# Kernel tuning notes

Hardware: AMD Instinct MI355X
Metric: run time of the kernel (lower is better)

The kernel has to match this reference:

```python
import jax, jax.numpy as jnp
import numpy as np

B, T, F, U, L = 64, 512, 256, 1024, 3
LN_EPS = 1e-12  # tf.contrib.layers.layer_norm default


def setup_inputs() -> dict:
    key = jax.random.key(0)
    ks = jax.random.split(key, 8)

    def w(k, shape):
        return jax.random.normal(k, shape, jnp.float32) / np.float32(np.sqrt(shape[0]))

    return {
        "input": jax.random.normal(ks[0], (B, T, F), jnp.float32),
        "conditioned_lst": jax.random.randint(ks[1], (T,), 0, 2).astype(bool),
        # LSTM layer 0: input = feature F, layers 1..2: input = U
        "W0": w(ks[2], (F + U, 4 * U)), "b0": jnp.zeros((4 * U,), jnp.float32),
        "W1": w(ks[3], (2 * U, 4 * U)), "b1": jnp.zeros((4 * U,), jnp.float32),
        "W2": w(ks[4], (2 * U, 4 * U)), "b2": jnp.zeros((4 * U,), jnp.float32),
        # output dense projection back to feature dim
        "Wd": w(ks[5], (U, F)), "bd": jnp.zeros((F,), jnp.float32),
        # layer norm params
        "gamma": jnp.ones((F,), jnp.float32), "beta": jnp.zeros((F,), jnp.float32),
    }


def _lstm_cell(x, h, c, W, b):
    # BasicLSTMCell: gates in (i, j, f, o) order, forget_bias = 1.0
    z = jnp.dot(jnp.concatenate([x, h], axis=-1), W) + b
    i, j, f, o = jnp.split(z, 4, axis=-1)
    c_new = c * jax.nn.sigmoid(f + 1.0) + jax.nn.sigmoid(i) * jnp.tanh(j)
    h_new = jax.nn.sigmoid(o) * jnp.tanh(c_new)
    return h_new, c_new


def reference(input, conditioned_lst, W0, b0, W1, b1, W2, b2, Wd, bd, gamma, beta):
    Ws, bs = [W0, W1, W2], [b0, b1, b2]
    xs = (jnp.arange(T), jnp.swapaxes(input, 0, 1), conditioned_lst)  # time-major
    carry0 = (jnp.zeros((L, B, U), input.dtype),  # h per layer
              jnp.zeros((L, B, U), input.dtype),  # c per layer
              jnp.zeros((B, F), input.dtype))     # previous emit

    def step(carry, xt):
        hs, cs, prev_emit = carry
        t, x_t, cond_t = xt
        # auto-conditioning: teacher-force on conditioned steps (and step 0)
        x = jnp.where(jnp.logical_or(t == 0, cond_t), x_t, prev_emit)
        new_h, new_c = [], []
        for l in range(L):
            h, c = _lstm_cell(x, hs[l], cs[l], Ws[l], bs[l])
            new_h.append(h)
            new_c.append(c)
            x = h
        y = jnp.dot(x, Wd) + bd  # dense projection [B, F]
        mu = jnp.mean(y, axis=-1, keepdims=True)
        var = jnp.mean(jnp.square(y - mu), axis=-1, keepdims=True)
        y = (y - mu) * jax.lax.rsqrt(var + LN_EPS) * gamma + beta
        emit = jax.nn.relu(y)
        return (jnp.stack(new_h), jnp.stack(new_c), emit), emit

    _, outs = jax.lax.scan(step, carry0, xs)  # [T, B, F]
    return jnp.swapaxes(outs, 0, 1)  # [B, T, F]
```

## Files before the change

### kernel.cpp

```cpp
#include <hip/hip_runtime.h>
#include <math.h>

#define B 64
#define T 512
#define F 256
#define U 1024
#define NBLK 256
#define NTH 512
#define WPAD 68

typedef unsigned short ushort_t;
typedef __attribute__((ext_vector_type(8))) _Float16 f16x8_t;
typedef __attribute__((ext_vector_type(4))) float f32x4_t;

static const size_t OFF_STATS= 0;
static const size_t OFF_COND = 4096;
static const size_t OFF_BAR  = 6144;
static const size_t OFF_H2B  = 7424;
static const size_t OFF_HS   = 269568;
static const size_t OFF_XS   = 1056000;
static const size_t OFF_PW0  = 1088768;
static const size_t OFF_PW1  = 11574528;
static const size_t OFF_PW2  = 28351744;
static const size_t ZERO_BYTES = OFF_PW0;

__device__ __forceinline__ float sigm(float x) {
    return 1.0f / (1.0f + __expf(-x));
}

__device__ __forceinline__ ushort_t f2h(float x) {
    _Float16 h = (_Float16)x;
    union { _Float16 h; ushort_t u; } v; v.h = h;
    return v.u;
}

__device__ __forceinline__ void store_uc_u16(ushort_t* p, ushort_t v) {
    asm volatile("global_store_short %0, %1, off sc0 sc1"
                 :: "v"(p), "v"((unsigned)v) : "memory");
}
__device__ __forceinline__ void store_uc_f32(float* p, float v) {
    asm volatile("global_store_dword %0, %1, off sc0 sc1"
                 :: "v"(p), "v"(v) : "memory");
}
__device__ __forceinline__ void store_uc_b64(void* p, unsigned long long v) {
    asm volatile("global_store_dwordx2 %0, %1, off sc0 sc1"
                 :: "v"(p), "v"(v) : "memory");
}
__device__ __forceinline__ void drain_vmem() {
    asm volatile("s_waitcnt vmcnt(0)" ::: "memory");
}
__device__ __forceinline__ void wait_vm0() {
    asm volatile("s_waitcnt vmcnt(0)" ::: "memory");
    __builtin_amdgcn_sched_barrier(0);
}

__device__ __forceinline__ void phase_sync(int* bar, int epoch, int g) {
    drain_vmem();
    __syncthreads();
    if (threadIdx.x == 0) {
        const int sub = g & 7;
        const int prev = __hip_atomic_fetch_add(bar + sub * 16, 1,
                                                __ATOMIC_RELAXED, __HIP_MEMORY_SCOPE_AGENT);
        if (prev == epoch * 32 - 1) {
            const int pm = __hip_atomic_fetch_add(bar + 128, 1,
                                                  __ATOMIC_RELAXED, __HIP_MEMORY_SCOPE_AGENT);
            if (pm == epoch * 8 - 1) {
                #pragma unroll
                for (int i = 0; i < 8; ++i)
                    __hip_atomic_store(bar + 144 + i * 16, epoch, __ATOMIC_RELAXED,
                                       __HIP_MEMORY_SCOPE_AGENT);
            }
        }
        int* myrelay = bar + 144 + sub * 16;
        int spins = 0;
        while (__hip_atomic_load(myrelay, __ATOMIC_RELAXED,
                                 __HIP_MEMORY_SCOPE_AGENT) < epoch) {
            __builtin_amdgcn_s_sleep(2);
            if ((++spins & 63) == 0)
                (void)__hip_atomic_load(myrelay, __ATOMIC_ACQUIRE,
                                        __HIP_MEMORY_SCOPE_AGENT);
        }
    }
    __syncthreads();
}

__global__ void prep_kernel(const unsigned char* __restrict__ condraw,
                            const float* __restrict__ input,
                            unsigned char* __restrict__ wsb) {
    __shared__ int s_not_int32;
    const int tid = threadIdx.x;
    if (tid == 0) s_not_int32 = 0;
    __syncthreads();
    if (tid < 512 && (tid & 3) != 0) {
        if (condraw[tid] != 0) s_not_int32 = 1;
    }
    __syncthreads();
    const int is32 = (s_not_int32 == 0);
    int* condw = (int*)(wsb + OFF_COND);
    if (tid < 512) {
        int cv = is32 ? ((const int*)condraw)[tid] : (int)condraw[tid];
        condw[tid] = (cv != 0) ? 1 : 0;
    }
    ushort_t* xs = (ushort_t*)(wsb + OFF_XS);
    for (int i = tid; i < B * F; i += blockDim.x) {
        const int b = i >> 8, f = i & 255;
        xs[(size_t)(((f >> 2) << 6) + b) * 4 + (f & 3)] =
            f2h(input[(size_t)b * (T * F) + f]);
    }
}

__global__ void repack_kernel(const float* __restrict__ W0,
                              const float* __restrict__ W1,
                              const float* __restrict__ W2,
                              unsigned char* __restrict__ wsb) {
    ushort_t* P0 = (ushort_t*)(wsb + OFF_PW0);
    ushort_t* P1 = (ushort_t*)(wsb + OFF_PW1);
    ushort_t* P2 = (ushort_t*)(wsb + OFF_PW2);
    const size_t stride = (size_t)gridDim.x * blockDim.x;
    const size_t tid = (size_t)blockIdx.x * blockDim.x + threadIdx.x;
    const size_t N0 = (size_t)256 * 40 * 512;
    const size_t N12 = (size_t)256 * 64 * 512;
    for (size_t i = tid; i < N0; i += stride) {
        const int g = (int)(i / 20480);
        const int r = (int)(i % 20480);
        const int kt = r >> 9, s = r & 511, L = s >> 3, j = s & 7;
        const int k = kt * 32 + ((L >> 4) << 3) + j;
        const int n = L & 15;
        const int col = ((n >> 2) << 10) + (g << 2) + (n & 3);
        P0[i] = f2h(W0[(size_t)k * 4096 + col]);
    }
    for (size_t i = tid; i < N12; i += stride) {
        const int g = (int)(i / 32768);
        const int r = (int)(i % 32768);
        const int kt = r >> 9, s = r & 511, L = s >> 3, j = s & 7;
        const int k = kt * 32 + ((L >> 4) << 3) + j;
        const int n = L & 15;
        const int col = ((n >> 2) << 10) + (g << 2) + (n & 3);
        const size_t src = (size_t)k * 4096 + col;
        P1[i] = f2h(W1[src]);
        P2[i] = f2h(W2[src]);
    }
}

__global__ void __launch_bounds__(NTH, 2)
lstm_persistent(const float* __restrict__ input,
                const float* __restrict__ b0, const float* __restrict__ b1,
                const float* __restrict__ b2,
                const float* __restrict__ Wd, const float* __restrict__ bd,
                const float* __restrict__ gamma, const float* __restrict__ beta,
                float* __restrict__ out, unsigned char* __restrict__ wsb) {
    const int g = blockIdx.x;
    const int tid = threadIdx.x;
    const int lane = tid & 63;
    const int wv = __builtin_amdgcn_readfirstlane(tid >> 6);
    const int ln15 = lane & 15;
    const int quad = lane >> 4;

    float* h2b = (float*)(wsb + OFF_H2B);
    float* stats = (float*)(wsb + OFF_STATS);
    int* bar = (int*)(wsb + OFF_BAR);
    ushort_t* hs = (ushort_t*)(wsb + OFF_HS);
    ushort_t* xs = (ushort_t*)(wsb + OFF_XS);
    const size_t HSZ = (size_t)256 * 64 * 4;

    __shared__ f16x8_t lds_pw0[40 * 64];
    __shared__ f32x4_t lds_wd4[1024];
    __shared__ float zbuf[128 * WPAD];
    __shared__ int lds_cond[512];

    const int u0 = g << 2;
    const int f0 = g << 2;

    f16x8_t Bw1[8], Bw2[8];
    {
        const ushort_t* p1 = (const ushort_t*)(wsb + OFF_PW1) +
                             (size_t)g * 64 * 512 + (size_t)lane * 8;
        const ushort_t* p2 = (const ushort_t*)(wsb + OFF_PW2) +
                             (size_t)g * 64 * 512 + (size_t)lane * 8;
        #pragma unroll
        for (int i = 0; i < 4; ++i) {
            Bw1[i]     = *(const f16x8_t*)(p1 + (size_t)((wv << 2) + i) * 512);
            Bw1[4 + i] = *(const f16x8_t*)(p1 + (size_t)(32 + (wv << 2) + i) * 512);
            Bw2[i]     = *(const f16x8_t*)(p2 + (size_t)((wv << 2) + i) * 512);
            Bw2[4 + i] = *(const f16x8_t*)(p2 + (size_t)(32 + (wv << 2) + i) * 512);
        }
    }
    {
        const f16x8_t* src = (const f16x8_t*)((const ushort_t*)(wsb + OFF_PW0) +
                                              (size_t)g * 40 * 512);
        for (int i = tid; i < 40 * 64; i += NTH) lds_pw0[i] = src[i];
    }
    if (g < 64) {
        for (int k = tid; k < 1024; k += NTH)
            lds_wd4[k] = *(const f32x4_t*)(Wd + (size_t)k * F + f0);
    }
    for (int i = tid; i < 512; i += NTH) lds_cond[i] = ((const int*)(wsb + OFF_COND))[i];

    const int eb = tid & 63;
    const int eu = (tid >> 6) & 3;

    float bias0[4], bias1[4], bias2[4];
    if (tid < 256) {
        #pragma unroll
        for (int q = 0; q < 4; ++q) {
            bias0[q] = b0[(q << 10) + u0 + eu];
            bias1[q] = b1[(q << 10) + u0 + eu];
            bias2[q] = b2[(q << 10) + u0 + eu];
        }
    }
    float4 gm4 = {0,0,0,0}, bt4 = {0,0,0,0}, bd4 = {0,0,0,0};
    if (g < 64 && wv == 0) {
        gm4 = *(const float4*)(gamma + f0);
        bt4 = *(const float4*)(beta + f0);
        bd4 = *(const float4*)(bd + f0);
    }
    __syncthreads();

    float creg0 = 0.f, creg1 = 0.f, creg2 = 0.f;

    f32x4_t acc0[4], acc1[4], acc2[4];
    #pragma unroll
    for (int mt = 0; mt < 4; ++mt) {
        acc0[mt] = (f32x4_t){0.f, 0.f, 0.f, 0.f};
        acc1[mt] = (f32x4_t){0.f, 0.f, 0.f, 0.f};
        acc2[mt] = (f32x4_t){0.f, 0.f, 0.f, 0.f};
    }

    auto ld_frag = [&](const char* p) -> f16x8_t {
        union { unsigned long long q[2]; f16x8_t v; } u;
        u.q[0] = *(const unsigned long long*)(p);
        u.q[1] = *(const unsigned long long*)(p + 512);
        return u.v;
    };

    auto mm4 = [&](f32x4_t (&acc)[4], const ushort_t* base,
                   const f16x8_t (&Bw)[8], const int boff) {
        f16x8_t Ab[4][4];
        const char* bb = (const char*)base + (size_t)ln15 * 8 +
                         (size_t)(quad << 1) * 512;
        #pragma unroll
        for (int c = 0; c < 4; ++c) {
            const char* pc = bb + (size_t)((wv << 2) + c) * 4096;
            #pragma unroll
            for (int mt = 0; mt < 4; ++mt)
                Ab[c][mt] = ld_frag(pc + mt * 128);
        }
        #pragma unroll
        for (int c = 0; c < 4; ++c) {
            #pragma unroll
            for (int mt = 0; mt < 4; ++mt)
                acc[mt] = __builtin_amdgcn_mfma_f32_16x16x32_f16(
                    Ab[c][mt], Bw[boff + c], acc[mt], 0, 0, 0);
        }
    };

    auto mm_h0 = [&](f32x4_t (&acc)[4], const ushort_t* base) {
        f16x8_t Ab[4][4];
        const char* bb = (const char*)base + (size_t)ln15 * 8 +
                         (size_t)(quad << 1) * 512;
        #pragma unroll
        for (int c = 0; c < 4; ++c) {
            const char* pc = bb + (size_t)((wv << 2) + c) * 4096;
            #pragma unroll
            for (int mt = 0; mt < 4; ++mt)
                Ab[c][mt] = ld_frag(pc + mt * 128);
        }
        #pragma unroll
        for (int c = 0; c < 4; ++c) {
            const f16x8_t Bb = lds_pw0[(8 + (wv << 2) + c) * 64 + lane];
            #pragma unroll
            for (int mt = 0; mt < 4; ++mt)
                acc[mt] = __builtin_amdgcn_mfma_f32_16x16x32_f16(
                    Ab[c][mt], Bb, acc[mt], 0, 0, 0);
        }
    };

    auto epilogue = [&](f32x4_t (&acc)[4], const float (&bi)[4], float& cr,
                        ushort_t* hdst, float* h2dst) {
        __syncthreads();
        {
            float* zrow = zbuf + (size_t)(wv * 16 + ln15) * WPAD;
            #pragma unroll
            for (int mt = 0; mt < 4; ++mt)
                *(f32x4_t*)(zrow + mt * 16 + (quad << 2)) = acc[mt];
            #pragma unroll
            for (int mt = 0; mt < 4; ++mt) acc[mt] = (f32x4_t){0.f, 0.f, 0.f, 0.f};
        }
        __syncthreads();
        if (tid < 256) {
            float z[4];
            #pragma unroll
            for (int q = 0; q < 4; ++q) {
                float s = bi[q];
                #pragma unroll
                for (int w = 0; w < 8; ++w)
                    s += zbuf[(size_t)(w * 16 + q * 4 + eu) * WPAD + eb];
                z[q] = s;
            }
            const float ig = sigm(z[0]);
            const float gg = tanhf(z[1]);
            const float fg = sigm(z[2] + 1.0f);
            const float og = sigm(z[3]);
            const float cn = cr * fg + ig * gg;
            const float hn = og * tanhf(cn);
            cr = cn;
            store_uc_u16(hdst + ((size_t)g * 64 + eb) * 4 + eu, f2h(hn));
            if (h2dst) store_uc_f32(h2dst + ((size_t)g * 64 + eb) * 4 + eu, hn);
        }
    };

    int epoch = 0;
    for (int t = 0; t < T; ++t) {
        const int p = t & 1;
        const int pn = p ^ 1;
        ushort_t* hs0n = hs + (size_t)(pn * 3 + 0) * HSZ;
        ushort_t* hs1n = hs + (size_t)(pn * 3 + 1) * HSZ;
        ushort_t* hs2n = hs + (size_t)(pn * 3 + 2) * HSZ;

        __builtin_amdgcn_fence(__ATOMIC_ACQUIRE, "agent");

        if (g < 64) {
            mm4(acc1, hs + (size_t)(p * 3 + 1) * HSZ, Bw1, 4);
            mm4(acc2, hs + (size_t)(p * 3 + 2) * HSZ, Bw2, 4);
        }
        {
            f16x8_t Ax[4];
            const char* bb = (const char*)xs + (size_t)ln15 * 8 +
                             (size_t)(quad << 1) * 512 + (size_t)wv * 4096;
            #pragma unroll
            for (int mt = 0; mt < 4; ++mt)
                Ax[mt] = ld_frag(bb + mt * 128);
            const f16x8_t Bb = lds_pw0[wv * 64 + lane];
            #pragma unroll
            for (int mt = 0; mt < 4; ++mt)
                acc0[mt] = __builtin_amdgcn_mfma_f32_16x16x32_f16(
                    Ax[mt], Bb, acc0[mt], 0, 0, 0);
        }
        epilogue(acc0, bias0, creg0, hs0n, nullptr);
        phase_sync(bar, ++epoch, g);

        mm4(acc1, hs0n, Bw1, 0);
        if (g < 64) mm_h0(acc0, hs0n);
        epilogue(acc1, bias1, creg1, hs1n, nullptr);
        phase_sync(bar, ++epoch, g);

        mm4(acc2, hs1n, Bw2, 0);
        epilogue(acc2, bias2, creg2, hs2n, h2b);
        phase_sync(bar, ++epoch, g);

        if (g < 64) {
            float accd[4] = {0.f, 0.f, 0.f, 0.f};
            #pragma unroll
            for (int half = 0; half < 2; ++half) {
                f32x4_t hv[16];
                const f32x4_t* hb4 = (const f32x4_t*)h2b +
                    (size_t)(wv * 32 + half * 16) * 64 + lane;
                #pragma unroll
                for (int i = 0; i < 16; ++i)
                    hv[i] = hb4[(size_t)i * 64];
                #pragma unroll
                for (int i = 0; i < 16; ++i) {
                    const int k = (wv << 7) + (half << 6) + (i << 2);
                    #pragma unroll
                    for (int j = 0; j < 4; ++j) {
                        const f32x4_t w4 = lds_wd4[k + j];
                        accd[0] = fmaf(w4[0], hv[i][j], accd[0]);
                        accd[1] = fmaf(w4[1], hv[i][j], accd[1]);
                        accd[2] = fmaf(w4[2], hv[i][j], accd[2]);
                        accd[3] = fmaf(w4[3], hv[i][j], accd[3]);
                    }
                }
            }
            __syncthreads();
            #pragma unroll
            for (int jj = 0; jj < 4; ++jj)
                zbuf[(size_t)(wv * 16 + jj) * WPAD + lane] = accd[jj];
            __syncthreads();
            if (wv == 0) {
                float yv[4];
                float s = 0.f, ss = 0.f;
                #pragma unroll
                for (int jj = 0; jj < 4; ++jj) {
                    float y = 0.f;
                    #pragma unroll
                    for (int w = 0; w < 8; ++w)
                        y += zbuf[(size_t)(w * 16 + jj) * WPAD + lane];
                    y += (jj == 0) ? bd4.x : (jj == 1) ? bd4.y : (jj == 2) ? bd4.z : bd4.w;
                    yv[jj] = y;
                    s += y;
                    ss += y * y;
                }
                float* st = stats + (size_t)p * (64 * 8);
                atomicAdd(&st[(size_t)lane * 8], s);
                atomicAdd(&st[(size_t)lane * 8 + 1], ss);
                if (lane == 0) {
                    drain_vmem();
                    __hip_atomic_fetch_add(bar + 272, 1, __ATOMIC_RELAXED,
                                           __HIP_MEMORY_SCOPE_AGENT);
                    const int target = (t + 1) * 64;
                    int spins = 0;
                    while (__hip_atomic_load(bar + 272, __ATOMIC_RELAXED,
                                             __HIP_MEMORY_SCOPE_AGENT) < target) {
                        __builtin_amdgcn_s_sleep(2);
                        if ((++spins & 63) == 0)
                            (void)__hip_atomic_load(bar + 272, __ATOMIC_ACQUIRE,
                                                    __HIP_MEMORY_SCOPE_AGENT);
                    }
                }
                union { unsigned long long u64; float f[2]; } sv;
                asm volatile("global_load_dwordx2 %0, %1, off sc0 sc1"
                             : "=v"(sv.u64) : "v"(st + (size_t)lane * 8));
                wait_vm0();
                const float mu = sv.f[0] * (1.0f / F);
                const float var = sv.f[1] * (1.0f / F) - mu * mu;
                const float rs = rsqrtf(var + 1e-12f);
                float em[4];
                em[0] = fmaxf((yv[0] - mu) * rs * gm4.x + bt4.x, 0.0f);
                em[1] = fmaxf((yv[1] - mu) * rs * gm4.y + bt4.y, 0.0f);
                em[2] = fmaxf((yv[2] - mu) * rs * gm4.z + bt4.z, 0.0f);
                em[3] = fmaxf((yv[3] - mu) * rs * gm4.w + bt4.w, 0.0f);
                *(float4*)(out + (size_t)lane * (T * F) + (size_t)t * F + f0) =
                    make_float4(em[0], em[1], em[2], em[3]);
                if (t + 1 < T) {
                    float xn[4];
                    if (lds_cond[t + 1] != 0) {
                        const float4 iv = *(const float4*)(input + (size_t)lane * (T * F) +
                                                           (size_t)(t + 1) * F + f0);
                        xn[0] = iv.x; xn[1] = iv.y; xn[2] = iv.z; xn[3] = iv.w;
                    } else {
                        xn[0] = em[0]; xn[1] = em[1]; xn[2] = em[2]; xn[3] = em[3];
                    }
                    unsigned long long pk =
                        (unsigned long long)f2h(xn[0]) |
                        ((unsigned long long)f2h(xn[1]) << 16) |
                        ((unsigned long long)f2h(xn[2]) << 32) |
                        ((unsigned long long)f2h(xn[3]) << 48);
                    store_uc_b64(xs + ((size_t)g * 64 + lane) * 4, pk);
                }
            }
        } else if (g == 64 && wv == 0) {
            float* st2 = stats + (size_t)pn * (64 * 8);
            store_uc_b64(&st2[(size_t)lane * 8], 0ULL);
        }

        if (g >= 64 && t + 1 < T) {
            mm_h0(acc0, hs0n);
            mm4(acc1, hs1n, Bw1, 4);
            mm4(acc2, hs2n, Bw2, 4);
        }
        phase_sync(bar, ++epoch, g);
    }
}

extern "C" void kernel_launch(void* const* d_in, const int* in_sizes, int n_in,
                              void* d_out, int out_size, void* d_ws, size_t ws_size,
                              hipStream_t stream) {
    const float* input = (const float*)d_in[0];
    const unsigned char* condraw = (const unsigned char*)d_in[1];
    const float* W0 = (const float*)d_in[2];
    const float* b0 = (const float*)d_in[3];
    const float* W1 = (const float*)d_in[4];
    const float* b1 = (const float*)d_in[5];
    const float* W2 = (const float*)d_in[6];
    const float* b2 = (const float*)d_in[7];
    const float* Wd = (const float*)d_in[8];
    const float* bd = (const float*)d_in[9];
    const float* gamma = (const float*)d_in[10];
    const float* beta = (const float*)d_in[11];
    float* out = (float*)d_out;
    unsigned char* wsb = (unsigned char*)d_ws;

    hipMemsetAsync(d_ws, 0, ZERO_BYTES, stream);
    prep_kernel<<<1, 512, 0, stream>>>(condraw, input, wsb);
    repack_kernel<<<2048, 256, 0, stream>>>(W0, W1, W2, wsb);
    lstm_persistent<<<NBLK, NTH, 0, stream>>>(input, b0, b1, b2, Wd, bd,
                                              gamma, beta, out, wsb);
}
```

Before: 24.15 ms.

## Defer layer-norm finalization to next step, removing mid-step dense-stats spin barrier

```diff
diff --git a/kernel.cpp b/kernel.cpp
--- a/kernel.cpp
+++ b/kernel.cpp
@@ -18,7 +18,7 @@
 static const size_t OFF_BAR  = 6144;
 static const size_t OFF_H2B  = 7424;
 static const size_t OFF_HS   = 269568;
-static const size_t OFF_XS   = 1056000;
+static const size_t OFF_YB   = 1056000;
 static const size_t OFF_PW0  = 1088768;
 static const size_t OFF_PW1  = 11574528;
 static const size_t OFF_PW2  = 28351744;
@@ -33,6 +33,10 @@
     union { _Float16 h; ushort_t u; } v; v.h = h;
     return v.u;
 }
+__device__ __forceinline__ float h2f(ushort_t u) {
+    union { ushort_t u; _Float16 h; } v; v.u = u;
+    return (float)v.h;
+}
 
 __device__ __forceinline__ void store_uc_u16(ushort_t* p, ushort_t v) {
     asm volatile("global_store_short %0, %1, off sc0 sc1"
@@ -48,10 +52,6 @@
 }
 __device__ __forceinline__ void drain_vmem() {
     asm volatile("s_waitcnt vmcnt(0)" ::: "memory");
-}
-__device__ __forceinline__ void wait_vm0() {
-    asm volatile("s_waitcnt vmcnt(0)" ::: "memory");
-    __builtin_amdgcn_sched_barrier(0);
 }
 
 __device__ __forceinline__ void phase_sync(int* bar, int epoch, int g) {
@@ -75,8 +75,8 @@
         int spins = 0;
         while (__hip_atomic_load(myrelay, __ATOMIC_RELAXED,
                                  __HIP_MEMORY_SCOPE_AGENT) < epoch) {
-            __builtin_amdgcn_s_sleep(2);
-            if ((++spins & 63) == 0)
+            __builtin_amdgcn_s_sleep(1);
+            if ((++spins & 255) == 0)
                 (void)__hip_atomic_load(myrelay, __ATOMIC_ACQUIRE,
                                         __HIP_MEMORY_SCOPE_AGENT);
         }
@@ -85,7 +85,6 @@
 }
 
 __global__ void prep_kernel(const unsigned char* __restrict__ condraw,
-                            const float* __restrict__ input,
                             unsigned char* __restrict__ wsb) {
     __shared__ int s_not_int32;
     const int tid = threadIdx.x;
@@ -100,12 +99,6 @@
     if (tid < 512) {
         int cv = is32 ? ((const int*)condraw)[tid] : (int)condraw[tid];
         condw[tid] = (cv != 0) ? 1 : 0;
-    }
-    ushort_t* xs = (ushort_t*)(wsb + OFF_XS);
-    for (int i = tid; i < B * F; i += blockDim.x) {
-        const int b = i >> 8, f = i & 255;
-        xs[(size_t)(((f >> 2) << 6) + b) * 4 + (f & 3)] =
-            f2h(input[(size_t)b * (T * F) + f]);
     }
 }
 
@@ -160,16 +153,19 @@
     float* stats = (float*)(wsb + OFF_STATS);
     int* bar = (int*)(wsb + OFF_BAR);
     ushort_t* hs = (ushort_t*)(wsb + OFF_HS);
-    ushort_t* xs = (ushort_t*)(wsb + OFF_XS);
+    ushort_t* yb = (ushort_t*)(wsb + OFF_YB);
     const size_t HSZ = (size_t)256 * 64 * 4;
 
     __shared__ f16x8_t lds_pw0[40 * 64];
     __shared__ f32x4_t lds_wd4[1024];
     __shared__ float zbuf[128 * WPAD];
+    __shared__ float zbuf2[128];
     __shared__ int lds_cond[512];
 
     const int u0 = g << 2;
     const int f0 = g << 2;
+    const int k0 = (wv << 5) + (quad << 3);
+    const int fb0 = k0 >> 2;
 
     f16x8_t Bw1[8], Bw2[8];
     {
@@ -196,8 +192,8 @@
     }
     for (int i = tid; i < 512; i += NTH) lds_cond[i] = ((const int*)(wsb + OFF_COND))[i];
 
-    const int eb = tid & 63;
-    const int eu = (tid >> 6) & 3;
+    const int eb = tid >> 2;
+    const int eu = tid & 3;
 
     float bias0[4], bias1[4], bias2[4];
     if (tid < 256) {
@@ -208,10 +204,23 @@
             bias2[q] = b2[(q << 10) + u0 + eu];
         }
     }
+    float gmv[8], btv[8];
+    {
+        const float4 g0 = *(const float4*)(gamma + k0);
+        const float4 g1 = *(const float4*)(gamma + k0 + 4);
+        const float4 t0 = *(const float4*)(beta + k0);
+        const float4 t1 = *(const float4*)(beta + k0 + 4);
+        gmv[0]=g0.x; gmv[1]=g0.y; gmv[2]=g0.z; gmv[3]=g0.w;
+        gmv[4]=g1.x; gmv[5]=g1.y; gmv[6]=g1.z; gmv[7]=g1.w;
+        btv[0]=t0.x; btv[1]=t0.y; btv[2]=t0.z; btv[3]=t0.w;
+        btv[4]=t1.x; btv[5]=t1.y; btv[6]=t1.z; btv[7]=t1.w;
+    }
     float4 gm4 = {0,0,0,0}, bt4 = {0,0,0,0}, bd4 = {0,0,0,0};
-    if (g < 64 && wv == 0) {
+    if (g < 64 && wv == 1) {
         gm4 = *(const float4*)(gamma + f0);
         bt4 = *(const float4*)(beta + f0);
+    }
+    if (g < 64 && wv == 0) {
         bd4 = *(const float4*)(bd + f0);
     }
     __syncthreads();
@@ -304,8 +313,8 @@
             const float cn = cr * fg + ig * gg;
             const float hn = og * tanhf(cn);
             cr = cn;
-            store_uc_u16(hdst + ((size_t)g * 64 + eb) * 4 + eu, f2h(hn));
-            if (h2dst) store_uc_f32(h2dst + ((size_t)g * 64 + eb) * 4 + eu, hn);
+            store_uc_u16(hdst + (size_t)g * 256 + tid, f2h(hn));
+            if (h2dst) store_uc_f32(h2dst + (size_t)g * 256 + tid, hn);
         }
     };
 
@@ -323,13 +332,53 @@
             mm4(acc1, hs + (size_t)(p * 3 + 1) * HSZ, Bw1, 4);
             mm4(acc2, hs + (size_t)(p * 3 + 2) * HSZ, Bw2, 4);
         }
+        if (tid < 64) {
+            const float2 sv = *(const float2*)(stats + (size_t)pn * (64 * 8) + tid * 8);
+            const float mu = sv.x * (1.0f / F);
+            const float var = sv.y * (1.0f / F) - mu * mu;
+            zbuf2[tid * 2] = mu;
+            zbuf2[tid * 2 + 1] = rsqrtf(var + 1e-12f);
+        }
+        __syncthreads();
+        if (g < 64 && wv == 1 && t > 0) {
+            union { unsigned long long q; ushort_t s[4]; } yq;
+            yq.q = *(const unsigned long long*)(yb + ((size_t)g * 64 + lane) * 4);
+            const float mu = zbuf2[lane * 2], rs = zbuf2[lane * 2 + 1];
+            float4 o;
+            o.x = fmaxf((h2f(yq.s[0]) - mu) * rs * gm4.x + bt4.x, 0.0f);
+            o.y = fmaxf((h2f(yq.s[1]) - mu) * rs * gm4.y + bt4.y, 0.0f);
+            o.z = fmaxf((h2f(yq.s[2]) - mu) * rs * gm4.z + bt4.z, 0.0f);
+            o.w = fmaxf((h2f(yq.s[3]) - mu) * rs * gm4.w + bt4.w, 0.0f);
+            *(float4*)(out + (size_t)lane * (T * F) + (size_t)(t - 1) * F + f0) = o;
+        }
         {
+            const int condt = (t == 0) || (lds_cond[t] != 0);
             f16x8_t Ax[4];
-            const char* bb = (const char*)xs + (size_t)ln15 * 8 +
-                             (size_t)(quad << 1) * 512 + (size_t)wv * 4096;
-            #pragma unroll
-            for (int mt = 0; mt < 4; ++mt)
-                Ax[mt] = ld_frag(bb + mt * 128);
+            #pragma unroll
+            for (int mt = 0; mt < 4; ++mt) {
+                const int b = ln15 + (mt << 4);
+                union { ushort_t s[8]; f16x8_t v; } ux;
+                if (condt) {
+                    const float* ip = input + (size_t)b * (T * F) + (size_t)t * F + k0;
+                    const float4 a0 = *(const float4*)(ip);
+                    const float4 a1 = *(const float4*)(ip + 4);
+                    ux.s[0] = f2h(a0.x); ux.s[1] = f2h(a0.y);
+                    ux.s[2] = f2h(a0.z); ux.s[3] = f2h(a0.w);
+                    ux.s[4] = f2h(a1.x); ux.s[5] = f2h(a1.y);
+                    ux.s[6] = f2h(a1.z); ux.s[7] = f2h(a1.w);
+                } else {
+                    union { unsigned long long q; ushort_t s[4]; } y0, y1;
+                    y0.q = *(const unsigned long long*)(yb + ((size_t)fb0 * 64 + b) * 4);
+                    y1.q = *(const unsigned long long*)(yb + ((size_t)(fb0 + 1) * 64 + b) * 4);
+                    const float mu = zbuf2[b * 2], rs = zbuf2[b * 2 + 1];
+                    #pragma unroll
+                    for (int j = 0; j < 4; ++j) {
+                        ux.s[j] = f2h(fmaxf((h2f(y0.s[j]) - mu) * rs * gmv[j] + btv[j], 0.0f));
+                        ux.s[4 + j] = f2h(fmaxf((h2f(y1.s[j]) - mu) * rs * gmv[4 + j] + btv[4 + j], 0.0f));
+                    }
+                }
+                Ax[mt] = ux.v;
+            }
             const f16x8_t Bb = lds_pw0[wv * 64 + lane];
             #pragma unroll
             for (int mt = 0; mt < 4; ++mt)
@@ -390,53 +439,15 @@
                     s += y;
                     ss += y * y;
                 }
+                unsigned long long pk =
+                    (unsigned long long)f2h(yv[0]) |
+                    ((unsigned long long)f2h(yv[1]) << 16) |
+                    ((unsigned long long)f2h(yv[2]) << 32) |
+                    ((unsigned long long)f2h(yv[3]) << 48);
+                store_uc_b64(yb + ((size_t)g * 64 + lane) * 4, pk);
                 float* st = stats + (size_t)p * (64 * 8);
                 atomicAdd(&st[(size_t)lane * 8], s);
                 atomicAdd(&st[(size_t)lane * 8 + 1], ss);
-                if (lane == 0) {
-                    drain_vmem();
-                    __hip_atomic_fetch_add(bar + 272, 1, __ATOMIC_RELAXED,
-                                           __HIP_MEMORY_SCOPE_AGENT);
-                    const int target = (t + 1) * 64;
-                    int spins = 0;
-                    while (__hip_atomic_load(bar + 272, __ATOMIC_RELAXED,
-                                             __HIP_MEMORY_SCOPE_AGENT) < target) {
-                        __builtin_amdgcn_s_sleep(2);
-                        if ((++spins & 63) == 0)
-                            (void)__hip_atomic_load(bar + 272, __ATOMIC_ACQUIRE,
-                                                    __HIP_MEMORY_SCOPE_AGENT);
-                    }
-                }
-                union { unsigned long long u64; float f[2]; } sv;
-                asm volatile("global_load_dwordx2 %0, %1, off sc0 sc1"
-                             : "=v"(sv.u64) : "v"(st + (size_t)lane * 8));
-                wait_vm0();
-                const float mu = sv.f[0] * (1.0f / F);
-                const float var = sv.f[1] * (1.0f / F) - mu * mu;
-                const float rs = rsqrtf(var + 1e-12f);
-                float em[4];
-                em[0] = fmaxf((yv[0] - mu) * rs * gm4.x + bt4.x, 0.0f);
-                em[1] = fmaxf((yv[1] - mu) * rs * gm4.y + bt4.y, 0.0f);
-                em[2] = fmaxf((yv[2] - mu) * rs * gm4.z + bt4.z, 0.0f);
-                em[3] = fmaxf((yv[3] - mu) * rs * gm4.w + bt4.w, 0.0f);
-                *(float4*)(out + (size_t)lane * (T * F) + (size_t)t * F + f0) =
-                    make_float4(em[0], em[1], em[2], em[3]);
-                if (t + 1 < T) {
-                    float xn[4];
-                    if (lds_cond[t + 1] != 0) {
-                        const float4 iv = *(const float4*)(input + (size_t)lane * (T * F) +
-                                                           (size_t)(t + 1) * F + f0);
-                        xn[0] = iv.x; xn[1] = iv.y; xn[2] = iv.z; xn[3] = iv.w;
-                    } else {
-                        xn[0] = em[0]; xn[1] = em[1]; xn[2] = em[2]; xn[3] = em[3];
-                    }
-                    unsigned long long pk =
-                        (unsigned long long)f2h(xn[0]) |
-                        ((unsigned long long)f2h(xn[1]) << 16) |
-                        ((unsigned long long)f2h(xn[2]) << 32) |
-                        ((unsigned long long)f2h(xn[3]) << 48);
-                    store_uc_b64(xs + ((size_t)g * 64 + lane) * 4, pk);
-                }
             }
         } else if (g == 64 && wv == 0) {
             float* st2 = stats + (size_t)pn * (64 * 8);
@@ -449,6 +460,29 @@
             mm4(acc2, hs2n, Bw2, 4);
         }
         phase_sync(bar, ++epoch, g);
+    }
+
+    if (g < 64) {
+        __builtin_amdgcn_fence(__ATOMIC_ACQUIRE, "agent");
+        if (tid < 64) {
+            const float2 sv = *(const float2*)(stats + (size_t)((T - 1) & 1) * (64 * 8) + tid * 8);
+            const float mu = sv.x * (1.0f / F);
+            const float var = sv.y * (1.0f / F) - mu * mu;
+            zbuf2[tid * 2] = mu;
+            zbuf2[tid * 2 + 1] = rsqrtf(var + 1e-12f);
+        }
+        __syncthreads();
+        if (wv == 1) {
+            union { unsigned long long q; ushort_t s[4]; } yq;
+            yq.q = *(const unsigned long long*)(yb + ((size_t)g * 64 + lane) * 4);
+            const float mu = zbuf2[lane * 2], rs = zbuf2[lane * 2 + 1];
+            float4 o;
+            o.x = fmaxf((h2f(yq.s[0]) - mu) * rs * gm4.x + bt4.x, 0.0f);
+            o.y = fmaxf((h2f(yq.s[1]) - mu) * rs * gm4.y + bt4.y, 0.0f);
+            o.z = fmaxf((h2f(yq.s[2]) - mu) * rs * gm4.z + bt4.z, 0.0f);
+            o.w = fmaxf((h2f(yq.s[3]) - mu) * rs * gm4.w + bt4.w, 0.0f);
+            *(float4*)(out + (size_t)lane * (T * F) + (size_t)(T - 1) * F + f0) = o;
+        }
     }
 }
 
@@ -471,7 +505,7 @@
     unsigned char* wsb = (unsigned char*)d_ws;
 
     hipMemsetAsync(d_ws, 0, ZERO_BYTES, stream);
-    prep_kernel<<<1, 512, 0, stream>>>(condraw, input, wsb);
+    prep_kernel<<<1, 512, 0, stream>>>(condraw, wsb);
     repack_kernel<<<2048, 256, 0, stream>>>(W0, W1, W2, wsb);
     lstm_persistent<<<NBLK, NTH, 0, stream>>>(input, b0, b1, b2, Wd, bd,
                                               gamma, beta, out, wsb);
```

Result: slower. 25.59 ms (+6.0%).
